# Kernel tuning notes

Hardware: AMD Instinct MI355X
Metric: run time of the kernel (lower is better)

## Reference

```python
import jax, jax.numpy as jnp
import numpy as np

EMBED_DIM = 4096
NUM_HEADS = 32
HEAD_DIM = EMBED_DIM // NUM_HEADS  # 128
SEQ_LEN = HEAD_DIM // 2            # 64, forced by the module's RoPE broadcasting
BATCH = 32
W_SCALE = 0.01


def _rope(x, t):
    # Faithful to the original (including its unusual 'bij,d->bidj' axis layout).
    # x: (b, h, s, d); t: (s,)
    d = x.shape[-1]
    inv_freq = 1.0 / (10000.0 ** (jnp.arange(0, d, 2, dtype=jnp.float32) / d))  # (d//2,)
    t3 = t.astype(jnp.float32)[None, None, :]            # (1, 1, s)
    freqs = jnp.einsum('bij,d->bidj', t3, inv_freq)      # (1, 1, d//2, s)
    emb = jnp.concatenate([freqs, freqs], axis=-1)       # (1, 1, d//2, 2s) == (1,1,s,d) since s=d//2
    half = d // 2
    x_rot = jnp.concatenate([-x[..., half:], x[..., :half]], axis=-1)
    return x * jnp.cos(emb) + x_rot * jnp.sin(emb)


def setup_inputs() -> dict:
    key = jax.random.key(0)
    ks = jax.random.split(key, 11)
    e = EMBED_DIM
    def w(k):
        return jax.random.normal(k, (e, e), jnp.float32) * W_SCALE
    def b(k):
        return jax.random.normal(k, (e,), jnp.float32) * W_SCALE
    return {
        'x': jax.random.normal(ks[0], (BATCH, SEQ_LEN, e), jnp.float32),
        't': jnp.arange(SEQ_LEN, dtype=jnp.float32),
        'Wq': w(ks[1]), 'bq': b(ks[2]),
        'Wk': w(ks[3]), 'bk': b(ks[4]),
        'Wv': w(ks[5]), 'bv': b(ks[6]),
        'Wd': w(ks[7]), 'bd': b(ks[8]),
        'Wo': w(ks[9]), 'bo': b(ks[10]),
    }


def reference(x, t, Wq, bq, Wk, bk, Wv, bv, Wd, bd, Wo, bo):
    bsz, s, e = x.shape
    h, d = NUM_HEADS, HEAD_DIM

    def proj(W, bias):
        return (x @ W.T + bias).reshape(bsz, s, h, d).transpose(0, 2, 1, 3)  # (b,h,s,d)

    Q = _rope(proj(Wq, bq), t)
    K = _rope(proj(Wk, bk), t)
    V = proj(Wv, bv)

    gamma = jax.nn.sigmoid(x @ Wd.T + bd).reshape(bsz, s, h, d).transpose(0, 2, 1, 3)
    gc = jnp.cumprod(gamma, axis=2)  # (b,h,s,d), cumprod over sequence
    # mean_d(gc[q,:]/gc[k,:]) == (gc @ (1/gc)^T)/d -- same math as the original's
    # (b,h,q,k,d) D_full.mean(-1), without materializing the rank-5 tensor.
    D_mean = jnp.einsum('bhqd,bhkd->bhqk', gc, 1.0 / gc) / d
    mask = jnp.tril(jnp.ones((s, s), x.dtype))  # causal mask (applied post-mean, same as pre-mean)

    scores = jnp.einsum('bhqd,bhkd->bhqk', Q, K)
    decayed = scores * D_mean * mask
    out = jnp.einsum('bhqk,bhkd->bhqd', decayed, V)  # (b,h,s,d)
    out = out.transpose(0, 2, 1, 3).reshape(bsz, s, e)
    return out @ Wo.T + bo
```

## Files before the change

### kernel.cpp

```cpp
#include <hip/hip_runtime.h>
#include <hip/hip_bf16.h>
#include <cstdint>
#include <cstddef>

typedef __bf16 bf16_t;
typedef __bf16 bf16x4 __attribute__((ext_vector_type(4)));
typedef __bf16 bf16x8 __attribute__((ext_vector_type(8)));
typedef float f32x4 __attribute__((ext_vector_type(4)));

#define D_EMB   4096
#define N_HEADS 32
#define HEAD_D  128
#define SEQ     64
#define NBATCH  32
#define MTOT    2048
#define MB      1048576ULL
#define N4X     2097152
#define N4W     4194304

__global__ __launch_bounds__(256) void cvt_all(
    const float* __restrict__ x,  const float* __restrict__ w0,
    const float* __restrict__ w1, const float* __restrict__ w2,
    const float* __restrict__ w3, const float* __restrict__ w4,
    bf16_t* __restrict__ xb, bf16_t* __restrict__ d0, bf16_t* __restrict__ d1,
    bf16_t* __restrict__ d2, bf16_t* __restrict__ d3, bf16_t* __restrict__ d4) {
  const int i = blockIdx.x * 256 + threadIdx.x;
  const float* s; bf16_t* d; int j;
  if (i < N4X) { s = x; d = xb; j = i; }
  else {
    const int r = i - N4X;
    const int wi = r >> 22;
    j = r & (N4W - 1);
    if (wi == 0)      { s = w0; d = d0; }
    else if (wi == 1) { s = w1; d = d1; }
    else if (wi == 2) { s = w2; d = d2; }
    else if (wi == 3) { s = w3; d = d3; }
    else              { s = w4; d = d4; }
  }
  const float4 v = ((const float4*)s)[j];
  bf16x4 o;
  o[0] = (bf16_t)v.x; o[1] = (bf16_t)v.y; o[2] = (bf16_t)v.z; o[3] = (bf16_t)v.w;
  ((bf16x4*)d)[j] = o;
}

__device__ __forceinline__ void lds_async16(void* lds, const void* gp) {
  __builtin_amdgcn_global_load_lds(
      (const __attribute__((address_space(1))) void*)gp,
      (__attribute__((address_space(3))) void*)lds, 16, 0, 0);
}

#define BARRIER() asm volatile("s_barrier" ::: "memory")
#define WAIT_LGKM0()                                          \
  do {                                                        \
    asm volatile("s_waitcnt lgkmcnt(0)" ::: "memory");        \
    __builtin_amdgcn_sched_barrier(0);                        \
  } while (0)
#define WAIT_VM(n) asm volatile("s_waitcnt vmcnt(" #n ")" ::: "memory")


#define READ_A(Q)                                                           \
  do {                                                                      \
    _Pragma("unroll")                                                       \
    for (int mi = 0; mi < 2; ++mi) {                                        \
      _Pragma("unroll")                                                     \
      for (int ks = 0; ks < 2; ++ks) {                                      \
        afr[mi][ks] =                                                       \
            *(const bf16x8*)(As + aoff + ((Q) * 2 + mi) * 1024 + ks * 16384); \
      }                                                                     \
    }                                                                       \
  } while (0)

#define MFMA_PHASE(Q)                                                       \
  do {                                                                      \
    __builtin_amdgcn_s_setprio(1);                                          \
    _Pragma("unroll")                                                       \
    for (int mi = 0; mi < 2; ++mi) {                                        \
      _Pragma("unroll")                                                     \
      for (int j = 0; j < 4; ++j) {                                         \
        _Pragma("unroll")                                                   \
        for (int ks = 0; ks < 2; ++ks) {                                    \
          acc[(Q) * 2 + mi][j] = __builtin_amdgcn_mfma_f32_16x16x32_bf16(   \
              afr[mi][ks], bfr[j][ks], acc[(Q) * 2 + mi][j], 0, 0, 0);      \
        }                                                                   \
      }                                                                     \
    }                                                                       \
    __builtin_amdgcn_s_setprio(0);                                          \
  } while (0)

__global__ __launch_bounds__(512, 2) void proj_gemm8(
    const bf16_t* __restrict__ x,
    const bf16_t* __restrict__ Wq, const float* __restrict__ bq,
    const bf16_t* __restrict__ Wk, const float* __restrict__ bk,
    const bf16_t* __restrict__ Wv, const float* __restrict__ bv_,
    const bf16_t* __restrict__ Wd, const float* __restrict__ bd,
    bf16_t* __restrict__ Qp, bf16_t* __restrict__ Kp,
    bf16_t* __restrict__ Vp, bf16_t* __restrict__ Gp) {
  __shared__ __align__(16) char smem[131072];

  const int tid  = threadIdx.x;
  const int lane = tid & 63;
  const int wave = tid >> 6;
  const int quad = lane >> 4, l16 = lane & 15;
  const int wm = wave >> 2, wn = wave & 3;

  const int bid = (int)blockIdx.x;
  const int sw  = ((bid & 7) << 6) | (bid >> 3);
  const int mt  = sw & 7;
  const int nt  = sw >> 3;
  const int m0  = mt << 8;
  const int mat = nt >> 4;
  const int n0  = (nt & 15) << 8;

  const bf16_t* Bw; const float* bias; bf16_t* dst;
  if (mat == 0)      { Bw = Wq; bias = bq;  dst = Qp; }
  else if (mat == 1) { Bw = Wk; bias = bk;  dst = Kp; }
  else if (mat == 2) { Bw = Wv; bias = bv_; dst = Vp; }
  else               { Bw = Wd; bias = bd;  dst = Gp; }

  const int p0 = tid * 16, p1 = p0 + 8192;
  const int o0 = p0 ^ (((p0 >> 7) & 3) << 4);
  const int o1 = p1 ^ (((p1 >> 7) & 3) << 4);
  const char* gA0 = (const char*)(x  + (size_t)(m0 + (o0 >> 6)) * D_EMB) + (o0 & 63);
  const char* gA1 = (const char*)(x  + (size_t)(m0 + (o1 >> 6)) * D_EMB) + (o1 & 63);
  const char* gB0 = (const char*)(Bw + (size_t)(n0 + (o0 >> 6)) * D_EMB) + (o0 & 63);
  const char* gB1 = (const char*)(Bw + (size_t)(n0 + (o1 >> 6)) * D_EMB) + (o1 & 63);

  auto stageA = [&](int nb, int ks, int kbyte) {
    char* d = smem + nb * 65536 + ks * 16384;
    lds_async16(d + p0, gA0 + kbyte + ks * 64);
    lds_async16(d + p1, gA1 + kbyte + ks * 64);
  };
  auto stageB = [&](int nb, int ks, int kbyte) {
    char* d = smem + nb * 65536 + 32768 + ks * 16384;
    lds_async16(d + p0, gB0 + kbyte + ks * 64);
    lds_async16(d + p1, gB1 + kbyte + ks * 64);
  };

  const int qsw  = (quad << 4) ^ ((l16 & 6) << 3);
  const int aoff = (wm * 128 + l16) * 64 + qsw;
  const int boff = 32768 + (wn * 64 + l16) * 64 + qsw;

  f32x4 acc[8][4];
  const f32x4 zero = {0.f, 0.f, 0.f, 0.f};
#pragma unroll
  for (int i = 0; i < 8; ++i)
#pragma unroll
    for (int j = 0; j < 4; ++j) acc[i][j] = zero;

  stageA(0, 0, 0); stageA(0, 1, 0);
  stageB(0, 0, 0); stageB(0, 1, 0);
  stageB(1, 0, 128); stageB(1, 1, 128);
  WAIT_VM(4);
  BARRIER();

  bf16x8 bfr[4][2], afr[2][2];

#pragma unroll 1
  for (int T = 0; T < 64; ++T) {
    const int buf = T & 1;
    const char* As = smem + buf * 65536;
    const int kb1 = (T + 1) << 7;
    const int kb2 = (T + 2) << 7;

#pragma unroll
    for (int j = 0; j < 4; ++j)
#pragma unroll
      for (int ks = 0; ks < 2; ++ks)
        bfr[j][ks] = *(const bf16x8*)(As + boff + j * 1024 + ks * 16384);
    READ_A(0);
    if (T < 63) stageA(buf ^ 1, 0, kb1);
    BARRIER();
    WAIT_LGKM0();
    MFMA_PHASE(0);
    BARRIER();

    READ_A(1);
    if (T < 63) stageA(buf ^ 1, 1, kb1);
    if (T < 62) stageB(buf, 0, kb2);
    BARRIER();
    WAIT_LGKM0();
    MFMA_PHASE(1);
    BARRIER();

    READ_A(2);
    if (T < 62) stageB(buf, 1, kb2);
    BARRIER();
    WAIT_LGKM0();
    MFMA_PHASE(2);
    BARRIER();

    READ_A(3);
    BARRIER();
    WAIT_LGKM0();
    MFMA_PHASE(3);
    if (T < 62) { WAIT_VM(4); } else { WAIT_VM(0); }
    BARRIER();
  }

  const bool is_g = (mat == 3);
#pragma unroll
  for (int j = 0; j < 4; ++j) {
    const int col = n0 + wn * 64 + j * 16 + l16;
    const float bb = bias[col];
#pragma unroll
    for (int mi = 0; mi < 8; ++mi) {
      const int rowb = m0 + wm * 128 + mi * 16 + quad * 4;
#pragma unroll
      for (int r = 0; r < 4; ++r) {
        float v = acc[mi][j][r] + bb;
        if (is_g) v = 1.0f / (1.0f + __expf(-v));
        dst[(size_t)(rowb + r) * D_EMB + col] = (bf16_t)v;
      }
    }
  }
}

__device__ __forceinline__ void gemm_core_bt(const bf16_t* __restrict__ A,
                                             const bf16_t* __restrict__ B,
                                             int K, int m0, int n0,
                                             bf16_t* As, bf16_t* Bs,
                                             f32x4 acc[4][4]) {
  const int tid  = threadIdx.x;
  const int lane = tid & 63;
  const int wave = tid >> 6;
  const int quad = lane >> 4;
  const int l16  = lane & 15;
  const int wm   = (wave >> 1) * 64;
  const int wn   = (wave & 1) * 64;

  const int q0 = tid;
  const int q1 = tid + 256;
  const int r0 = q0 >> 2, c0 = (q0 & 3) * 8;
  const int r1 = q1 >> 2, c1 = (q1 & 3) * 8;

  const bf16_t* Arow0 = A + (size_t)(m0 + r0) * K + c0;
  const bf16_t* Arow1 = A + (size_t)(m0 + r1) * K + c1;
  const bf16_t* Brow0 = B + (size_t)(n0 + r0) * K + c0;
  const bf16_t* Brow1 = B + (size_t)(n0 + r1) * K + c1;

  for (int k0 = 0; k0 < K; k0 += 32) {
    lds_async16(As + q0 * 8, Arow0 + k0);
    lds_async16(As + q1 * 8, Arow1 + k0);
    lds_async16(Bs + q0 * 8, Brow0 + k0);
    lds_async16(Bs + q1 * 8, Brow1 + k0);
    __syncthreads();

    bf16x8 af[4], bfv[4];
#pragma unroll
    for (int i = 0; i < 4; i++)
      af[i] = *(const bf16x8*)&As[(wm + 16 * i + l16) * 32 + quad * 8];
#pragma unroll
    for (int j = 0; j < 4; j++)
      bfv[j] = *(const bf16x8*)&Bs[(wn + 16 * j + l16) * 32 + quad * 8];
#pragma unroll
    for (int i = 0; i < 4; i++)
#pragma unroll
      for (int j = 0; j < 4; j++)
        acc[i][j] = __builtin_amdgcn_mfma_f32_16x16x32_bf16(af[i], bfv[j],
                                                            acc[i][j], 0, 0, 0);
    __syncthreads();
  }
}

__global__ __launch_bounds__(256) void attn_kernel(
    const bf16_t* __restrict__ Qp, const bf16_t* __restrict__ Kp,
    const bf16_t* __restrict__ Vp, const bf16_t* __restrict__ Gp,
    const float* __restrict__ t, bf16_t* __restrict__ attn) {
  __shared__ __align__(16) char smem[65536];
  bf16_t* Qs  = (bf16_t*)smem;
  bf16_t* Ks  = (bf16_t*)(smem + 16384);
  bf16_t* Gs  = (bf16_t*)(smem + 32768);
  bf16_t* IGs = (bf16_t*)(smem + 49152);
  bf16_t* Ps  = (bf16_t*)(smem + 32768);
  bf16_t* Vt  = (bf16_t*)(smem + 32768 + 9216);

  const int tid = threadIdx.x;
  const int lane = tid & 63, wv = tid >> 6;
  const int quad = lane >> 4, l16 = lane & 15;
  const int b = blockIdx.x >> 5, h = blockIdx.x & 31;
  const size_t base = (size_t)(b * SEQ) * D_EMB + (size_t)h * HEAD_D;

  for (int idx = tid; idx < SEQ * HEAD_D; idx += 256) {
    const int s = idx >> 7, d = idx & 127;
    const float invf = __expf(-0.14391156831212787f * (float)s);
    const float theta = t[d & 63] * invf;
    float sn, cs;
    __sincosf(theta, &sn, &cs);
    const size_t po = base + (size_t)s * D_EMB;
    {
      const float v = (float)Qp[po + d];
      const float o = (float)Qp[po + (d ^ 64)];
      const float rot = (d < 64) ? -o : o;
      Qs[idx] = (bf16_t)(v * cs + rot * sn);
    }
    {
      const float v = (float)Kp[po + d];
      const float o = (float)Kp[po + (d ^ 64)];
      const float rot = (d < 64) ? -o : o;
      Ks[idx] = (bf16_t)(v * cs + rot * sn);
    }
  }
  if (tid < HEAD_D) {
    const int d = tid;
    float run = 1.0f;
    for (int s = 0; s < SEQ; s++) {
      run *= (float)Gp[base + (size_t)s * D_EMB + d];
      Gs[s * HEAD_D + d]  = (bf16_t)run;
      IGs[s * HEAD_D + d] = (bf16_t)(1.0f / run);
    }
  }
  __syncthreads();

  f32x4 Sa[4], Da[4];
  const f32x4 zero = {0.f, 0.f, 0.f, 0.f};
#pragma unroll
  for (int j = 0; j < 4; j++) { Sa[j] = zero; Da[j] = zero; }

  for (int k0 = 0; k0 < HEAD_D; k0 += 32) {
    const bf16x8 aq = *(const bf16x8*)&Qs[(wv * 16 + l16) * HEAD_D + quad * 8 + k0];
    const bf16x8 ag = *(const bf16x8*)&Gs[(wv * 16 + l16) * HEAD_D + quad * 8 + k0];
#pragma unroll
    for (int j = 0; j < 4; j++) {
      const bf16x8 bk = *(const bf16x8*)&Ks [(16 * j + l16) * HEAD_D + quad * 8 + k0];
      const bf16x8 bg = *(const bf16x8*)&IGs[(16 * j + l16) * HEAD_D + quad * 8 + k0];
      Sa[j] = __builtin_amdgcn_mfma_f32_16x16x32_bf16(aq, bk, Sa[j], 0, 0, 0);
      Da[j] = __builtin_amdgcn_mfma_f32_16x16x32_bf16(ag, bg, Da[j], 0, 0, 0);
    }
  }
  __syncthreads();

#pragma unroll
  for (int j = 0; j < 4; j++) {
#pragma unroll
    for (int r = 0; r < 4; r++) {
      const int q = wv * 16 + quad * 4 + r;
      const int k = 16 * j + l16;
      const float v = (k <= q) ? Sa[j][r] * Da[j][r] * 0.0078125f : 0.0f;
      Ps[q * 72 + k] = (bf16_t)v;
    }
  }
  for (int idx = tid; idx < SEQ * HEAD_D; idx += 256) {
    const int s = idx >> 7, d = idx & 127;
    Vt[d * 72 + s] = Vp[base + (size_t)s * D_EMB + d];
  }
  __syncthreads();

  f32x4 oa[8];
#pragma unroll
  for (int j = 0; j < 8; j++) oa[j] = zero;
  for (int k0 = 0; k0 < SEQ; k0 += 32) {
    const bf16x8 ap = *(const bf16x8*)&Ps[(wv * 16 + l16) * 72 + quad * 8 + k0];
#pragma unroll
    for (int j = 0; j < 8; j++) {
      const bf16x8 bv = *(const bf16x8*)&Vt[(16 * j + l16) * 72 + quad * 8 + k0];
      oa[j] = __builtin_amdgcn_mfma_f32_16x16x32_bf16(ap, bv, oa[j], 0, 0, 0);
    }
  }
#pragma unroll
  for (int j = 0; j < 8; j++) {
#pragma unroll
    for (int r = 0; r < 4; r++) {
      const int q = wv * 16 + quad * 4 + r;
      attn[(size_t)(b * SEQ + q) * D_EMB + (size_t)h * HEAD_D + 16 * j + l16] =
          (bf16_t)oa[j][r];
    }
  }
}

__global__ __launch_bounds__(256) void out_gemm(
    const bf16_t* __restrict__ A, const bf16_t* __restrict__ Wo,
    const float* __restrict__ bo, float* __restrict__ out) {
  __shared__ __align__(16) bf16_t As[128 * 32];
  __shared__ __align__(16) bf16_t Bs[128 * 32];

  const int m0 = blockIdx.x * 128;
  const int n0 = blockIdx.y * 128;

  f32x4 acc[4][4];
  const f32x4 zero = {0.f, 0.f, 0.f, 0.f};
#pragma unroll
  for (int i = 0; i < 4; i++)
#pragma unroll
    for (int j = 0; j < 4; j++) acc[i][j] = zero;

  gemm_core_bt(A, Wo, D_EMB, m0, n0, As, Bs, acc);

  const int tid = threadIdx.x, lane = tid & 63, wave = tid >> 6;
  const int quad = lane >> 4, l16 = lane & 15;
  const int wm = (wave >> 1) * 64, wn = (wave & 1) * 64;

#pragma unroll
  for (int i = 0; i < 4; i++) {
#pragma unroll
    for (int j = 0; j < 4; j++) {
      const int col = n0 + wn + 16 * j + l16;
      const float bv_ = bo[col];
      const int rowb = m0 + wm + 16 * i + quad * 4;
#pragma unroll
      for (int r = 0; r < 4; r++)
        out[(size_t)(rowb + r) * D_EMB + col] = acc[i][j][r] + bv_;
    }
  }
}

extern "C" void kernel_launch(void* const* d_in, const int* in_sizes, int n_in,
                              void* d_out, int out_size, void* d_ws, size_t ws_size,
                              hipStream_t stream) {
  const float* x  = (const float*)d_in[0];
  const float* t  = (const float*)d_in[1];
  const float* Wq = (const float*)d_in[2];
  const float* bq = (const float*)d_in[3];
  const float* Wk = (const float*)d_in[4];
  const float* bk = (const float*)d_in[5];
  const float* Wv = (const float*)d_in[6];
  const float* bv = (const float*)d_in[7];
  const float* Wd = (const float*)d_in[8];
  const float* bd = (const float*)d_in[9];
  const float* Wo = (const float*)d_in[10];
  const float* bo = (const float*)d_in[11];

  char* ws = (char*)d_ws;
  bf16_t* xb   = (bf16_t*)(ws);
  bf16_t* Wqb  = (bf16_t*)(ws + 16 * MB);
  bf16_t* Wkb  = (bf16_t*)(ws + 48 * MB);
  bf16_t* Wvb  = (bf16_t*)(ws + 80 * MB);
  bf16_t* Wdb  = (bf16_t*)(ws + 112 * MB);
  bf16_t* Wob  = (bf16_t*)(ws + 144 * MB);
  bf16_t* Qp   = (bf16_t*)(ws + 176 * MB);
  bf16_t* Kp   = (bf16_t*)(ws + 192 * MB);
  bf16_t* Vp   = (bf16_t*)(ws + 208 * MB);
  bf16_t* Gp   = (bf16_t*)(ws + 224 * MB);
  bf16_t* attn = (bf16_t*)(ws);

  const int nblk = (N4X + 5 * N4W) / 256;
  cvt_all<<<nblk, 256, 0, stream>>>(x, Wq, Wk, Wv, Wd, Wo,
                                    xb, Wqb, Wkb, Wvb, Wdb, Wob);
  proj_gemm8<<<dim3(512), 512, 0, stream>>>(xb, Wqb, bq, Wkb, bk, Wvb, bv,
                                            Wdb, bd, Qp, Kp, Vp, Gp);
  attn_kernel<<<dim3(1024), 256, 0, stream>>>(Qp, Kp, Vp, Gp, t, attn);
  out_gemm<<<dim3(16, 32), 256, 0, stream>>>(attn, Wob, bo, (float*)d_out);
}
```

Measured before the change: 757.1 us.

## Merge four MFMA phases into two per K-tile with double-buffered A fragments

Restructures the projection GEMM main loop from four LDS-read/MFMA phases per K-tile into two phases. Each phase now reads two A fragment sets into separate register arrays and issues the async global-to-LDS staging before running both MFMA blocks. This removes about half of the barriers and the explicit lgkmcnt waits, leaving the compiler to insert the waits. The cost is more live registers, and the schedule is less tightly interleaved, which could expose LDS latency or hurt occupancy at two blocks per CU.

```diff
diff --git a/kernel.cpp b/kernel.cpp
--- a/kernel.cpp
+++ b/kernel.cpp
@@ -50,29 +50,24 @@
 }
 
 #define BARRIER() asm volatile("s_barrier" ::: "memory")
-#define WAIT_LGKM0()                                          \
-  do {                                                        \
-    asm volatile("s_waitcnt lgkmcnt(0)" ::: "memory");        \
-    __builtin_amdgcn_sched_barrier(0);                        \
-  } while (0)
 #define WAIT_VM(n) asm volatile("s_waitcnt vmcnt(" #n ")" ::: "memory")
-
-
-#define READ_A(Q)                                                           \
+#define SCHED_FENCE() __builtin_amdgcn_sched_barrier(0)
+
+
+#define READ_AQ(DST, Q)                                                     \
   do {                                                                      \
     _Pragma("unroll")                                                       \
     for (int mi = 0; mi < 2; ++mi) {                                        \
       _Pragma("unroll")                                                     \
       for (int ks = 0; ks < 2; ++ks) {                                      \
-        afr[mi][ks] =                                                       \
+        DST[mi][ks] =                                                       \
             *(const bf16x8*)(As + aoff + ((Q) * 2 + mi) * 1024 + ks * 16384); \
       }                                                                     \
     }                                                                       \
   } while (0)
 
-#define MFMA_PHASE(Q)                                                       \
+#define MFMA_Q(Q, AFR)                                                      \
   do {                                                                      \
-    __builtin_amdgcn_s_setprio(1);                                          \
     _Pragma("unroll")                                                       \
     for (int mi = 0; mi < 2; ++mi) {                                        \
       _Pragma("unroll")                                                     \
@@ -80,11 +75,10 @@
         _Pragma("unroll")                                                   \
         for (int ks = 0; ks < 2; ++ks) {                                    \
           acc[(Q) * 2 + mi][j] = __builtin_amdgcn_mfma_f32_16x16x32_bf16(   \
-              afr[mi][ks], bfr[j][ks], acc[(Q) * 2 + mi][j], 0, 0, 0);      \
+              AFR[mi][ks], bfr[j][ks], acc[(Q) * 2 + mi][j], 0, 0, 0);      \
         }                                                                   \
       }                                                                     \
     }                                                                       \
-    __builtin_amdgcn_s_setprio(0);                                          \
   } while (0)
 
 __global__ __launch_bounds__(512, 2) void proj_gemm8(
@@ -153,7 +147,7 @@
   WAIT_VM(4);
   BARRIER();
 
-  bf16x8 bfr[4][2], afr[2][2];
+  bf16x8 bfr[4][2], afr0[2][2], afr1[2][2];
 
 #pragma unroll 1
   for (int T = 0; T < 64; ++T) {
@@ -167,32 +161,24 @@
 #pragma unroll
       for (int ks = 0; ks < 2; ++ks)
         bfr[j][ks] = *(const bf16x8*)(As + boff + j * 1024 + ks * 16384);
-    READ_A(0);
-    if (T < 63) stageA(buf ^ 1, 0, kb1);
+    READ_AQ(afr0, 0);
+    READ_AQ(afr1, 1);
+    if (T < 63) { stageA(buf ^ 1, 0, kb1); stageA(buf ^ 1, 1, kb1); }
+    __builtin_amdgcn_s_setprio(1);
+    MFMA_Q(0, afr0);
+    MFMA_Q(1, afr1);
+    __builtin_amdgcn_s_setprio(0);
+    SCHED_FENCE();
     BARRIER();
-    WAIT_LGKM0();
-    MFMA_PHASE(0);
-    BARRIER();
-
-    READ_A(1);
-    if (T < 63) stageA(buf ^ 1, 1, kb1);
-    if (T < 62) stageB(buf, 0, kb2);
-    BARRIER();
-    WAIT_LGKM0();
-    MFMA_PHASE(1);
-    BARRIER();
-
-    READ_A(2);
-    if (T < 62) stageB(buf, 1, kb2);
-    BARRIER();
-    WAIT_LGKM0();
-    MFMA_PHASE(2);
-    BARRIER();
-
-    READ_A(3);
-    BARRIER();
-    WAIT_LGKM0();
-    MFMA_PHASE(3);
+
+    READ_AQ(afr0, 2);
+    READ_AQ(afr1, 3);
+    if (T < 62) { stageB(buf, 0, kb2); stageB(buf, 1, kb2); }
+    __builtin_amdgcn_s_setprio(1);
+    MFMA_Q(2, afr0);
+    MFMA_Q(3, afr1);
+    __builtin_amdgcn_s_setprio(0);
+    SCHED_FENCE();
     if (T < 62) { WAIT_VM(4); } else { WAIT_VM(0); }
     BARRIER();
   }
```

Result: faster. 730.1 us (-3.6%).

## Reorder projection GEMM inner loop to hold A fragments and stream B per phase

Applied to the files above, without the earlier changes.

Restructures the main K loop of the projection GEMM so each wave loads all eight A fragments for one k-slice and reuses them across B fragment pairs, rather than loading all B and streaming A. The staging schedule changes so A is prefetched further ahead and B later, with the vmcnt wait threshold adjusted to match. The aim is to cut LDS read traffic and rebalance when global-to-LDS copies overlap with MFMA work. It risks higher register pressure and buffer reuse hazards from the new prefetch order.

```diff
diff --git a/kernel.cpp b/kernel.cpp
--- a/kernel.cpp
+++ b/kernel.cpp
@@ -50,42 +50,13 @@
 }
 
 #define BARRIER() asm volatile("s_barrier" ::: "memory")
+#define WAIT_VM(n) asm volatile("s_waitcnt vmcnt(" #n ")" ::: "memory")
 #define WAIT_LGKM0()                                          \
   do {                                                        \
     asm volatile("s_waitcnt lgkmcnt(0)" ::: "memory");        \
     __builtin_amdgcn_sched_barrier(0);                        \
   } while (0)
-#define WAIT_VM(n) asm volatile("s_waitcnt vmcnt(" #n ")" ::: "memory")
-
-
-#define READ_A(Q)                                                           \
-  do {                                                                      \
-    _Pragma("unroll")                                                       \
-    for (int mi = 0; mi < 2; ++mi) {                                        \
-      _Pragma("unroll")                                                     \
-      for (int ks = 0; ks < 2; ++ks) {                                      \
-        afr[mi][ks] =                                                       \
-            *(const bf16x8*)(As + aoff + ((Q) * 2 + mi) * 1024 + ks * 16384); \
-      }                                                                     \
-    }                                                                       \
-  } while (0)
-
-#define MFMA_PHASE(Q)                                                       \
-  do {                                                                      \
-    __builtin_amdgcn_s_setprio(1);                                          \
-    _Pragma("unroll")                                                       \
-    for (int mi = 0; mi < 2; ++mi) {                                        \
-      _Pragma("unroll")                                                     \
-      for (int j = 0; j < 4; ++j) {                                         \
-        _Pragma("unroll")                                                   \
-        for (int ks = 0; ks < 2; ++ks) {                                    \
-          acc[(Q) * 2 + mi][j] = __builtin_amdgcn_mfma_f32_16x16x32_bf16(   \
-              afr[mi][ks], bfr[j][ks], acc[(Q) * 2 + mi][j], 0, 0, 0);      \
-        }                                                                   \
-      }                                                                     \
-    }                                                                       \
-    __builtin_amdgcn_s_setprio(0);                                          \
-  } while (0)
+
 
 __global__ __launch_bounds__(512, 2) void proj_gemm8(
     const bf16_t* __restrict__ x,
@@ -149,11 +120,10 @@
 
   stageA(0, 0, 0); stageA(0, 1, 0);
   stageB(0, 0, 0); stageB(0, 1, 0);
-  stageB(1, 0, 128); stageB(1, 1, 128);
-  WAIT_VM(4);
+  stageA(1, 0, 128); stageA(1, 1, 128);
+  stageB(1, 0, 128);
+  WAIT_VM(6);
   BARRIER();
-
-  bf16x8 bfr[4][2], afr[2][2];
 
 #pragma unroll 1
   for (int T = 0; T < 64; ++T) {
@@ -162,38 +132,69 @@
     const int kb1 = (T + 1) << 7;
     const int kb2 = (T + 2) << 7;
 
-#pragma unroll
-    for (int j = 0; j < 4; ++j)
-#pragma unroll
-      for (int ks = 0; ks < 2; ++ks)
-        bfr[j][ks] = *(const bf16x8*)(As + boff + j * 1024 + ks * 16384);
-    READ_A(0);
-    if (T < 63) stageA(buf ^ 1, 0, kb1);
+    bf16x8 afr[8], b0, b1;
+
+#pragma unroll
+    for (int m8 = 0; m8 < 8; ++m8)
+      afr[m8] = *(const bf16x8*)(As + aoff + m8 * 1024);
+    b0 = *(const bf16x8*)(As + boff);
+    b1 = *(const bf16x8*)(As + boff + 1024);
+    if (T < 63) stageB(buf ^ 1, 1, kb1);
     BARRIER();
     WAIT_LGKM0();
-    MFMA_PHASE(0);
-    BARRIER();
-
-    READ_A(1);
-    if (T < 63) stageA(buf ^ 1, 1, kb1);
+    __builtin_amdgcn_s_setprio(1);
+#pragma unroll
+    for (int mi = 0; mi < 8; ++mi) {
+      acc[mi][0] = __builtin_amdgcn_mfma_f32_16x16x32_bf16(afr[mi], b0, acc[mi][0], 0, 0, 0);
+      acc[mi][1] = __builtin_amdgcn_mfma_f32_16x16x32_bf16(afr[mi], b1, acc[mi][1], 0, 0, 0);
+    }
+    __builtin_amdgcn_s_setprio(0);
+    BARRIER();
+
+    b0 = *(const bf16x8*)(As + boff + 2048);
+    b1 = *(const bf16x8*)(As + boff + 3072);
+    if (T < 62) stageA(buf, 0, kb2);
+    BARRIER();
+    WAIT_LGKM0();
+    __builtin_amdgcn_s_setprio(1);
+#pragma unroll
+    for (int mi = 0; mi < 8; ++mi) {
+      acc[mi][2] = __builtin_amdgcn_mfma_f32_16x16x32_bf16(afr[mi], b0, acc[mi][2], 0, 0, 0);
+      acc[mi][3] = __builtin_amdgcn_mfma_f32_16x16x32_bf16(afr[mi], b1, acc[mi][3], 0, 0, 0);
+    }
+    __builtin_amdgcn_s_setprio(0);
+    BARRIER();
+
+#pragma unroll
+    for (int m8 = 0; m8 < 8; ++m8)
+      afr[m8] = *(const bf16x8*)(As + aoff + m8 * 1024 + 16384);
+    b0 = *(const bf16x8*)(As + boff + 16384);
+    b1 = *(const bf16x8*)(As + boff + 16384 + 1024);
     if (T < 62) stageB(buf, 0, kb2);
     BARRIER();
     WAIT_LGKM0();
-    MFMA_PHASE(1);
-    BARRIER();
-
-    READ_A(2);
-    if (T < 62) stageB(buf, 1, kb2);
+    __builtin_amdgcn_s_setprio(1);
+#pragma unroll
+    for (int mi = 0; mi < 8; ++mi) {
+      acc[mi][0] = __builtin_amdgcn_mfma_f32_16x16x32_bf16(afr[mi], b0, acc[mi][0], 0, 0, 0);
+      acc[mi][1] = __builtin_amdgcn_mfma_f32_16x16x32_bf16(afr[mi], b1, acc[mi][1], 0, 0, 0);
+    }
+    __builtin_amdgcn_s_setprio(0);
+    BARRIER();
+
+    b0 = *(const bf16x8*)(As + boff + 16384 + 2048);
+    b1 = *(const bf16x8*)(As + boff + 16384 + 3072);
+    if (T < 62) stageA(buf, 1, kb2);
     BARRIER();
     WAIT_LGKM0();
-    MFMA_PHASE(2);
-    BARRIER();
-
-    READ_A(3);
-    BARRIER();
-    WAIT_LGKM0();
-    MFMA_PHASE(3);
-    if (T < 62) { WAIT_VM(4); } else { WAIT_VM(0); }
+    __builtin_amdgcn_s_setprio(1);
+#pragma unroll
+    for (int mi = 0; mi < 8; ++mi) {
+      acc[mi][2] = __builtin_amdgcn_mfma_f32_16x16x32_bf16(afr[mi], b0, acc[mi][2], 0, 0, 0);
+      acc[mi][3] = __builtin_amdgcn_mfma_f32_16x16x32_bf16(afr[mi], b1, acc[mi][3], 0, 0, 0);
+    }
+    __builtin_amdgcn_s_setprio(0);
+    if (T < 62) { WAIT_VM(6); } else { WAIT_VM(0); }
     BARRIER();
   }
 
```

Result: no change. 751.6 us (-0.7%).
